# Optimization experiments

Measured on AMD Instinct MI355X. Metric: run time of the kernel, lower is better.

The kernel has to match this reference:

```python
import jax, jax.numpy as jnp
import numpy as np

B, S, D = 16, 1024, 1024  # shape constraints force S == D == 1024


def setup_inputs() -> dict:
    key = jax.random.key(0)
    k1, k2, k3 = jax.random.split(key, 3)
    f1_norm = jax.random.normal(k1, (B, S, D), dtype=jnp.float32)
    f2_norm = jax.random.normal(k2, (B, S, D), dtype=jnp.float32)
    # xavier_normal_ init: std = sqrt(2 / (fan_in + fan_out))
    xavier_std = float(np.sqrt(2.0 / (D + D)))
    corr_weights = jax.random.normal(k3, (D, D), dtype=jnp.float32) * xavier_std
    return {"f1_norm": f1_norm, "f2_norm": f2_norm, "corr_weights": corr_weights}


def reference(f1_norm, f2_norm, corr_weights):
    # a1 = f1 @ W : [B, S, D]
    a1 = jnp.einsum('bsd,de->bse', f1_norm, corr_weights)
    # cc_mat = a1 @ f2^T : [B, S1, S2]
    cc_mat = jnp.einsum('bse,bte->bst', a1, f2_norm)
    audio_att = jax.nn.softmax(cc_mat, axis=1)                      # softmax over S1
    visual_att = jax.nn.softmax(jnp.swapaxes(cc_mat, 1, 2), axis=1)  # [B,S2,S1], softmax over S2
    atten_audiofeatures = jnp.matmul(f1_norm, audio_att)             # [B, S1(=D), S2]
    atten_visualfeatures = jnp.matmul(f2_norm, visual_att)           # [B, S2(=D), S1]
    return (jnp.swapaxes(atten_audiofeatures, 1, 2),
            jnp.swapaxes(atten_visualfeatures, 1, 2))
```

## Files before the change

### kernel.cpp

```cpp
#include <hip/hip_runtime.h>
#include <hip/hip_bf16.h>
#include <stdint.h>

typedef __bf16 bf16_t;
typedef bf16_t bf16x8 __attribute__((ext_vector_type(8)));
typedef bf16_t bf16x4 __attribute__((ext_vector_type(4)));
typedef float  f32x4  __attribute__((ext_vector_type(4)));

#define B_  16
#define S_  1024
#define D_  1024
#define BS_ (B_ * S_)
#define MAT_ (S_ * D_)

#define BAR()   __builtin_amdgcn_s_barrier()
#define LGKM0() asm volatile("s_waitcnt lgkmcnt(0)" ::: "memory")
#define VMC4()  asm volatile("s_waitcnt vmcnt(4)" ::: "memory")

__device__ __forceinline__ void async_load16(const void* g, void* l) {
    __builtin_amdgcn_global_load_lds((__attribute__((address_space(1))) void*)(g),
                                     (__attribute__((address_space(3))) void*)(l),
                                     16, 0, 0);
}

template <int SPLIT, int OSP, int XS>
__global__ __launch_bounds__(512, 2)
void gemm8p(const bf16_t* __restrict__ gAh, const bf16_t* __restrict__ gAl,
            const bf16_t* __restrict__ gBh, const bf16_t* __restrict__ gBl,
            float* __restrict__ Cf, bf16_t* __restrict__ Ch, bf16_t* __restrict__ Cl,
            int M, int N, int K, long sA, long sB, long sC)
{
    (void)M;
    constexpr int BK  = SPLIT ? 32 : 64;
    constexpr int BUF = 65536;
    __shared__ __attribute__((aligned(16))) char smem[2 * BUF];

    const int tid  = threadIdx.x;
    const int w    = tid >> 6;
    const int lane = tid & 63;
    const int wm   = w >> 2;
    const int wn   = w & 3;
    const int fm   = lane & 15;
    const int quad = lane >> 4;

    int bm, bn, b;
    if constexpr (XS) {
        const int flat = (int)blockIdx.x + ((int)blockIdx.y << 2) + ((int)blockIdx.z << 4);
        const int xcd = flat & 7, slot = flat >> 3;
        b  = (xcd << 1) | (slot >> 4);
        bm = (slot >> 2) & 3;
        bn = slot & 3;
    } else {
        bn = blockIdx.x; bm = blockIdx.y; b = blockIdx.z;
    }

    const int NT    = K / BK;
    const int abase = (int)((long)b * sA) + bm * 256 * K;
    const int bbase = (int)((long)b * sB) + bn * 256 * K;

    int aof[2][2], bof[2][2], lof[2][2];
    if constexpr (!SPLIT) {
#pragma unroll
        for (int h = 0; h < 2; ++h)
#pragma unroll
            for (int i = 0; i < 2; ++i) {
                const int o   = h * 16384 + i * 8192 + tid * 16;
                const int row = o >> 7;
                const int c   = ((o >> 4) & 7) ^ (((o >> 9) & 3) << 1);
                aof[h][i] = abase + row * K + c * 8;
                bof[h][i] = bbase + row * K + c * 8;
                lof[h][i] = o;
            }
    } else {
#pragma unroll
        for (int h = 0; h < 2; ++h) {
            const int o   = h * 8192 + tid * 16;
            const int row = o >> 6;
            const int c   = (o >> 4) & 3;
            aof[h][0] = abase + row * K + c * 8;
            bof[h][0] = bbase + row * K + c * 8;
            lof[h][0] = o;
        }
    }

    f32x4 acc[8][4] = {};

    if constexpr (!SPLIT) {
        auto stgA = [&](int t, int h, int lb) {
            const int k = (t < NT ? t : NT - 1) * BK;
            async_load16(gAh + (aof[h][0] + k), smem + lb + lof[h][0]);
            async_load16(gAh + (aof[h][1] + k), smem + lb + lof[h][1]);
        };
        auto stgB = [&](int t, int h, int lb) {
            const int k = (t < NT ? t : NT - 1) * BK;
            async_load16(gBh + (bof[h][0] + k), smem + lb + 32768 + lof[h][0]);
            async_load16(gBh + (bof[h][1] + k), smem + lb + 32768 + lof[h][1]);
        };
        const int xb = ((lane >> 2) & 3) << 5;
        auto ldA = [&](int lb, int m, int ks) -> bf16x8 {
            const int row = wm * 128 + m * 16 + fm;
            return *(const bf16x8*)(smem + lb + row * 128 + ((ks * 64 + quad * 16) ^ xb));
        };
        auto ldB = [&](int lb, int n, int ks) -> bf16x8 {
            const int row = wn * 64 + n * 16 + fm;
            return *(const bf16x8*)(smem + lb + 32768 + row * 128 + ((ks * 64 + quad * 16) ^ xb));
        };

        bf16x8 ar[4][2], br[4][2];
        auto qp = [&](int mh, int nh) {
#pragma unroll
            for (int m = 0; m < 4; ++m)
#pragma unroll
                for (int n = 0; n < 2; ++n) {
                    f32x4 c = acc[mh * 4 + m][nh * 2 + n];
                    c = __builtin_amdgcn_mfma_f32_16x16x32_bf16(ar[m][0], br[nh * 2 + n][0], c, 0, 0, 0);
                    c = __builtin_amdgcn_mfma_f32_16x16x32_bf16(ar[m][1], br[nh * 2 + n][1], c, 0, 0, 0);
                    acc[mh * 4 + m][nh * 2 + n] = c;
                }
        };

        stgA(0, 0, 0); stgA(0, 1, 0); stgB(0, 0, 0); stgB(0, 1, 0);
        stgB(1, 0, BUF); stgB(1, 1, BUF);
        VMC4(); BAR();

        const int NIT = NT >> 1;
        for (int it = 0; it < NIT; ++it) {
            const int t = it << 1;
#pragma unroll
            for (int ph = 0; ph < 2; ++ph) {
                const int rb = ph ? BUF : 0;
                const int ob = ph ? 0 : BUF;
                const int tt = t + ph;
#pragma unroll
                for (int m = 0; m < 4; ++m) { ar[m][0] = ldA(rb, m, 0); ar[m][1] = ldA(rb, m, 1); }
#pragma unroll
                for (int n = 0; n < 2; ++n) { br[n][0] = ldB(rb, n, 0); br[n][1] = ldB(rb, n, 1); }
                stgA(tt + 1, 0, ob);
                BAR(); LGKM0(); __builtin_amdgcn_s_setprio(1);
                qp(0, 0);
                __builtin_amdgcn_s_setprio(0); BAR();
#pragma unroll
                for (int n = 2; n < 4; ++n) { br[n][0] = ldB(rb, n, 0); br[n][1] = ldB(rb, n, 1); }
                stgA(tt + 1, 1, ob);
                BAR(); LGKM0(); __builtin_amdgcn_s_setprio(1);
                qp(0, 1);
                __builtin_amdgcn_s_setprio(0); BAR();
#pragma unroll
                for (int m = 0; m < 4; ++m) { ar[m][0] = ldA(rb, m + 4, 0); ar[m][1] = ldA(rb, m + 4, 1); }
                stgB(tt + 2, 0, rb);
                BAR(); LGKM0(); __builtin_amdgcn_s_setprio(1);
                qp(1, 0);
                __builtin_amdgcn_s_setprio(0); BAR();
                stgB(tt + 2, 1, rb);
                BAR(); LGKM0(); __builtin_amdgcn_s_setprio(1);
                qp(1, 1);
                __builtin_amdgcn_s_setprio(0); VMC4(); BAR();
            }
        }
    } else {
        auto stgAh = [&](int t, int lb) {
            const int k = (t < NT ? t : NT - 1) * BK;
            async_load16(gAh + (aof[0][0] + k), smem + lb + lof[0][0]);
            async_load16(gAh + (aof[1][0] + k), smem + lb + lof[1][0]);
        };
        auto stgAl = [&](int t, int lb) {
            const int k = (t < NT ? t : NT - 1) * BK;
            async_load16(gAl + (aof[0][0] + k), smem + lb + 16384 + lof[0][0]);
            async_load16(gAl + (aof[1][0] + k), smem + lb + 16384 + lof[1][0]);
        };
        auto stgBh = [&](int t, int lb) {
            const int k = (t < NT ? t : NT - 1) * BK;
            async_load16(gBh + (bof[0][0] + k), smem + lb + 32768 + lof[0][0]);
            async_load16(gBh + (bof[1][0] + k), smem + lb + 32768 + lof[1][0]);
        };
        auto stgBl = [&](int t, int lb) {
            const int k = (t < NT ? t : NT - 1) * BK;
            async_load16(gBl + (bof[0][0] + k), smem + lb + 49152 + lof[0][0]);
            async_load16(gBl + (bof[1][0] + k), smem + lb + 49152 + lof[1][0]);
        };
        auto ldSA = [&](int lb, int comp, int m) -> bf16x8 {
            const int row = wm * 128 + m * 16 + fm;
            return *(const bf16x8*)(smem + lb + comp * 16384 + row * 64 + quad * 16);
        };
        auto ldSB = [&](int lb, int comp, int n) -> bf16x8 {
            const int row = wn * 64 + n * 16 + fm;
            return *(const bf16x8*)(smem + lb + comp * 16384 + row * 64 + quad * 16);
        };

        bf16x8 arh[4], arl[4], brh[4], brl[4];
        auto qs = [&](int mh, int nh) {
#pragma unroll
            for (int m = 0; m < 4; ++m)
#pragma unroll
                for (int n = 0; n < 2; ++n) {
                    f32x4 c = acc[mh * 4 + m][nh * 2 + n];
                    c = __builtin_amdgcn_mfma_f32_16x16x32_bf16(arh[m], brh[nh * 2 + n], c, 0, 0, 0);
                    c = __builtin_amdgcn_mfma_f32_16x16x32_bf16(arl[m], brh[nh * 2 + n], c, 0, 0, 0);
                    c = __builtin_amdgcn_mfma_f32_16x16x32_bf16(arh[m], brl[nh * 2 + n], c, 0, 0, 0);
                    acc[mh * 4 + m][nh * 2 + n] = c;
                }
        };

        stgAh(0, 0); stgAl(0, 0); stgBh(0, 0); stgBl(0, 0);
        stgBh(1, BUF); stgBl(1, BUF);
        VMC4(); BAR();

        const int NIT = NT >> 1;
        for (int it = 0; it < NIT; ++it) {
            const int t = it << 1;
#pragma unroll
            for (int ph = 0; ph < 2; ++ph) {
                const int rb = ph ? BUF : 0;
                const int ob = ph ? 0 : BUF;
                const int tt = t + ph;
#pragma unroll
                for (int m = 0; m < 4; ++m) { arh[m] = ldSA(rb, 0, m); arl[m] = ldSA(rb, 1, m); }
#pragma unroll
                for (int n = 0; n < 2; ++n) { brh[n] = ldSB(rb, 2, n); brl[n] = ldSB(rb, 3, n); }
                stgAh(tt + 1, ob);
                BAR(); LGKM0(); __builtin_amdgcn_s_setprio(1);
                qs(0, 0);
                __builtin_amdgcn_s_setprio(0); BAR();
#pragma unroll
                for (int n = 2; n < 4; ++n) { brh[n] = ldSB(rb, 2, n); brl[n] = ldSB(rb, 3, n); }
                stgAl(tt + 1, ob);
                BAR(); LGKM0(); __builtin_amdgcn_s_setprio(1);
                qs(0, 1);
                __builtin_amdgcn_s_setprio(0); BAR();
#pragma unroll
                for (int m = 0; m < 4; ++m) { arh[m] = ldSA(rb, 0, m + 4); arl[m] = ldSA(rb, 1, m + 4); }
                stgBh(tt + 2, rb);
                BAR(); LGKM0(); __builtin_amdgcn_s_setprio(1);
                qs(1, 0);
                __builtin_amdgcn_s_setprio(0); BAR();
                stgBl(tt + 2, rb);
                BAR(); LGKM0(); __builtin_amdgcn_s_setprio(1);
                qs(1, 1);
                __builtin_amdgcn_s_setprio(0); VMC4(); BAR();
            }
        }
    }

#pragma unroll
    for (int i = 0; i < 8; ++i) {
        const int row0 = bm * 256 + wm * 128 + i * 16 + quad * 4;
#pragma unroll
        for (int j = 0; j < 4; ++j) {
            const int col = bn * 256 + wn * 64 + j * 16 + fm;
#pragma unroll
            for (int r = 0; r < 4; ++r) {
                const long idx = (long)b * sC + (long)(row0 + r) * N + col;
                const float v = acc[i][j][r];
                if constexpr (OSP) {
                    const bf16_t h = (bf16_t)v;
                    Ch[idx] = h;
                    Cl[idx] = (bf16_t)(v - (float)h);
                } else {
                    Cf[idx] = v;
                }
            }
        }
    }
}

__global__ void split_f32(const float* __restrict__ s,
                          bf16_t* __restrict__ h, bf16_t* __restrict__ l)
{
    const long i = ((long)blockIdx.x * 256 + threadIdx.x) * 4;
    float4 v = *(const float4*)(s + i);
    float a[4] = {v.x, v.y, v.z, v.w};
    bf16x4 hh, ll;
#pragma unroll
    for (int e = 0; e < 4; ++e) {
        const bf16_t hv = (bf16_t)a[e];
        hh[e] = hv;
        ll[e] = (bf16_t)(a[e] - (float)hv);
    }
    *(bf16x4*)(h + i) = hh;
    *(bf16x4*)(l + i) = ll;
}

__global__ void transpose_split_w(const float* __restrict__ W,
                                  bf16_t* __restrict__ Wth, bf16_t* __restrict__ Wtl)
{
    __shared__ float tile[32][33];
    const int d0 = blockIdx.x * 32, e0 = blockIdx.y * 32;
    const int tx = threadIdx.x, ty = threadIdx.y;
    for (int r = ty; r < 32; r += 8)
        tile[r][tx] = W[(long)(d0 + r) * D_ + e0 + tx];
    __syncthreads();
    for (int r = ty; r < 32; r += 8) {
        const float v = tile[tx][r];
        const bf16_t h = (bf16_t)v;
        Wth[(long)(e0 + r) * D_ + d0 + tx] = h;
        Wtl[(long)(e0 + r) * D_ + d0 + tx] = (bf16_t)(v - (float)h);
    }
}

__global__ void col_stats_partial(const float* __restrict__ cc,
                                  float* __restrict__ Mp, float* __restrict__ Zp)
{
    const int b = blockIdx.x, tc = blockIdx.y, sc = blockIdx.z;
    const int t = tc * 256 + threadIdx.x;
    const float* p = cc + (long)b * MAT_ + (long)sc * 128 * S_ + t;
    float m = p[0], z = 1.f;
    for (int s = 1; s < 128; ++s) {
        float v = p[(long)s * S_];
        float nm = fmaxf(m, v);
        z = z * __expf(m - nm) + __expf(v - nm);
        m = nm;
    }
    const int idx = ((b * 8 + sc) << 10) + t;
    Mp[idx] = m; Zp[idx] = z;
}

__global__ void col_stats_combine(const float* __restrict__ Mp, const float* __restrict__ Zp,
                                  float* __restrict__ Mst, float* __restrict__ Zst)
{
    const int i = blockIdx.x * 256 + threadIdx.x;
    const int b = i >> 10, t = i & 1023;
    float m = Mp[((b * 8) << 10) + t], z = Zp[((b * 8) << 10) + t];
    for (int c = 1; c < 8; ++c) {
        float mc = Mp[((b * 8 + c) << 10) + t];
        float zc = Zp[((b * 8 + c) << 10) + t];
        float nm = fmaxf(m, mc);
        z = z * __expf(m - nm) + zc * __expf(mc - nm);
        m = nm;
    }
    Mst[i] = m; Zst[i] = z;
}

__global__ void row_stats(const float* __restrict__ cc,
                          float* __restrict__ Nst, float* __restrict__ Yst)
{
    const int row  = (blockIdx.x * 256 + threadIdx.x) >> 6;
    const int lane = threadIdx.x & 63;
    const float* p = cc + (long)row * S_;
    float m = p[lane], z = 1.f;
    for (int j = 1; j < 16; ++j) {
        float v = p[lane + j * 64];
        float nm = fmaxf(m, v);
        z = z * __expf(m - nm) + __expf(v - nm);
        m = nm;
    }
    for (int off = 32; off > 0; off >>= 1) {
        float mo = __shfl_down(m, off);
        float zo = __shfl_down(z, off);
        float nm = fmaxf(m, mo);
        z = z * __expf(m - nm) + zo * __expf(mo - nm);
        m = nm;
    }
    if (lane == 0) { Nst[row] = m; Yst[row] = z; }
}

__global__ void build_atts(const float* __restrict__ cc,
                           const float* __restrict__ Mst, const float* __restrict__ Zst,
                           const float* __restrict__ Nst, const float* __restrict__ Yst,
                           bf16_t* __restrict__ attA, bf16_t* __restrict__ attV)
{
    __shared__ float tile[32][33];
    const int b = blockIdx.z;
    const int s0 = blockIdx.x * 32, t0 = blockIdx.y * 32;
    const int tx = threadIdx.x, ty = threadIdx.y;
    const float* src = cc + (long)b * MAT_;
    bf16_t* dV = attV + (long)b * MAT_;
    bf16_t* dA = attA + (long)b * MAT_;
    for (int r = ty; r < 32; r += 8) {
        const int s = s0 + r;
        const float v = src[(long)s * S_ + t0 + tx];
        tile[r][tx] = v;
        dV[(long)s * S_ + t0 + tx] =
            (bf16_t)(__expf(v - Nst[b * 1024 + s]) * (1.f / Yst[b * 1024 + s]));
    }
    __syncthreads();
    for (int r = ty; r < 32; r += 8) {
        const int t = t0 + r;
        const float m  = Mst[b * 1024 + t];
        const float rz = 1.f / Zst[b * 1024 + t];
        dA[(long)t * S_ + s0 + tx] = (bf16_t)(__expf(tile[tx][r] - m) * rz);
    }
}

extern "C" void kernel_launch(void* const* d_in, const int* in_sizes, int n_in,
                              void* d_out, int out_size, void* d_ws, size_t ws_size,
                              hipStream_t stream)
{
    const float* f1 = (const float*)d_in[0];
    const float* f2 = (const float*)d_in[1];
    const float* W  = (const float*)d_in[2];

    float* out0 = (float*)d_out;
    float* out1 = out0 + (long)B_ * MAT_;

    bf16_t* a1h = (bf16_t*)out0;
    bf16_t* a1l = a1h + (long)B_ * MAT_;
    bf16_t* Wth = (bf16_t*)out1;
    bf16_t* Wtl = Wth + (long)MAT_;
    float*  cc  = out1;

    char* w = (char*)d_ws;
    bf16_t* f1h  = (bf16_t*)(w);
    bf16_t* f2h  = (bf16_t*)(w + (32l << 20));
    bf16_t* f1l  = (bf16_t*)(w + (64l << 20));
    bf16_t* f2l  = (bf16_t*)(w + (96l << 20));
    bf16_t* attA = f1l;
    bf16_t* attV = f2l;
    float*  Mp   = (float*)(w + (128l << 20));
    float*  Zp   = Mp + 16 * 8 * 1024;
    float*  Mst  = Zp + 16 * 8 * 1024;
    float*  Zst  = Mst + BS_;
    float*  Nst  = Zst + BS_;
    float*  Yst  = Nst + BS_;

    split_f32<<<16384, 256, 0, stream>>>(f1, f1h, f1l);
    split_f32<<<16384, 256, 0, stream>>>(f2, f2h, f2l);
    transpose_split_w<<<dim3(32, 32), dim3(32, 8), 0, stream>>>(W, Wth, Wtl);

    gemm8p<1, 1, 0><<<dim3(4, 64, 1), 512, 0, stream>>>(
        f1h, f1l, Wth, Wtl, nullptr, a1h, a1l, BS_, 1024, 1024, 0, 0, 0);

    gemm8p<1, 0, 1><<<dim3(4, 4, 16), 512, 0, stream>>>(
        a1h, a1l, f2h, f2l, cc, nullptr, nullptr, 1024, 1024, 1024, MAT_, MAT_, MAT_);

    col_stats_partial<<<dim3(16, 4, 8), 256, 0, stream>>>(cc, Mp, Zp);
    col_stats_combine<<<64, 256, 0, stream>>>(Mp, Zp, Mst, Zst);
    row_stats<<<4096, 256, 0, stream>>>(cc, Nst, Yst);

    build_atts<<<dim3(32, 32, 16), dim3(32, 8), 0, stream>>>(
        cc, Mst, Zst, Nst, Yst, attA, attV);

    gemm8p<0, 0, 1><<<dim3(4, 4, 16), 512, 0, stream>>>(
        attA, nullptr, f1h, nullptr, out0, nullptr, nullptr,
        1024, 1024, 1024, MAT_, MAT_, MAT_);

    gemm8p<0, 0, 1><<<dim3(4, 4, 16), 512, 0, stream>>>(
        attV, nullptr, f2h, nullptr, out1, nullptr, nullptr,
        1024, 1024, 1024, MAT_, MAT_, MAT_);
}
```

Baseline: 565.2 us.

## Fuse softmax stats into GEMM epilogue, merge launches, and re-swizzle LDS

```diff
diff --git a/kernel.cpp b/kernel.cpp
--- a/kernel.cpp
+++ b/kernel.cpp
@@ -23,11 +23,13 @@
                                      16, 0, 0);
 }
 
-template <int SPLIT, int OSP, int XS>
+template <int SPLIT, int OSP, int XS, int STATS>
 __global__ __launch_bounds__(512, 2)
 void gemm8p(const bf16_t* __restrict__ gAh, const bf16_t* __restrict__ gAl,
             const bf16_t* __restrict__ gBh, const bf16_t* __restrict__ gBl,
             float* __restrict__ Cf, bf16_t* __restrict__ Ch, bf16_t* __restrict__ Cl,
+            float* __restrict__ Mp2, float* __restrict__ Zp2,
+            float* __restrict__ Np2, float* __restrict__ Yp2,
             int M, int N, int K, long sA, long sB, long sC)
 {
     (void)M;
@@ -44,14 +46,33 @@
     const int quad = lane >> 4;
 
     int bm, bn, b;
-    if constexpr (XS) {
+    if constexpr (XS == 1) {
         const int flat = (int)blockIdx.x + ((int)blockIdx.y << 2) + ((int)blockIdx.z << 4);
         const int xcd = flat & 7, slot = flat >> 3;
         b  = (xcd << 1) | (slot >> 4);
         bm = (slot >> 2) & 3;
         bn = slot & 3;
+    } else if constexpr (XS == 2) {
+        const int flat = (int)blockIdx.x + ((int)blockIdx.y << 2) + ((int)blockIdx.z << 4);
+        const int xcd = flat & 7, slot = flat >> 3;
+        b  = (xcd << 2) | (slot >> 4);
+        bm = (slot >> 2) & 3;
+        bn = slot & 3;
+    } else if constexpr (XS == 3) {
+        const int flat = (int)blockIdx.x + ((int)blockIdx.y << 2);
+        const int xcd = flat & 7, slot = flat >> 3;
+        b  = 0;
+        bm = (xcd << 3) | (slot >> 2);
+        bn = slot & 3;
     } else {
         bn = blockIdx.x; bm = blockIdx.y; b = blockIdx.z;
+    }
+
+    const bf16_t* pAh = gAh; const bf16_t* pAl = gAl;
+    const bf16_t* pBh = gBh; const bf16_t* pBl = gBl;
+    float* Cfp = Cf;
+    if constexpr (XS == 2) {
+        if (b >= 16) { pAh = gAl; pBh = gBl; Cfp = Cf + (long)B_ * MAT_; b -= 16; }
     }
 
     const int NT    = K / BK;
@@ -66,7 +87,7 @@
             for (int i = 0; i < 2; ++i) {
                 const int o   = h * 16384 + i * 8192 + tid * 16;
                 const int row = o >> 7;
-                const int c   = ((o >> 4) & 7) ^ (((o >> 9) & 3) << 1);
+                const int c   = ((o >> 4) & 7) ^ (row & 7);
                 aof[h][i] = abase + row * K + c * 8;
                 bof[h][i] = bbase + row * K + c * 8;
                 lof[h][i] = o;
@@ -76,7 +97,7 @@
         for (int h = 0; h < 2; ++h) {
             const int o   = h * 8192 + tid * 16;
             const int row = o >> 6;
-            const int c   = (o >> 4) & 3;
+            const int c   = ((o >> 4) & 3) ^ ((row >> 1) & 3);
             aof[h][0] = abase + row * K + c * 8;
             bof[h][0] = bbase + row * K + c * 8;
             lof[h][0] = o;
@@ -88,15 +109,15 @@
     if constexpr (!SPLIT) {
         auto stgA = [&](int t, int h, int lb) {
             const int k = (t < NT ? t : NT - 1) * BK;
-            async_load16(gAh + (aof[h][0] + k), smem + lb + lof[h][0]);
-            async_load16(gAh + (aof[h][1] + k), smem + lb + lof[h][1]);
+            async_load16(pAh + (aof[h][0] + k), smem + lb + lof[h][0]);
+            async_load16(pAh + (aof[h][1] + k), smem + lb + lof[h][1]);
         };
         auto stgB = [&](int t, int h, int lb) {
             const int k = (t < NT ? t : NT - 1) * BK;
-            async_load16(gBh + (bof[h][0] + k), smem + lb + 32768 + lof[h][0]);
-            async_load16(gBh + (bof[h][1] + k), smem + lb + 32768 + lof[h][1]);
-        };
-        const int xb = ((lane >> 2) & 3) << 5;
+            async_load16(pBh + (bof[h][0] + k), smem + lb + 32768 + lof[h][0]);
+            async_load16(pBh + (bof[h][1] + k), smem + lb + 32768 + lof[h][1]);
+        };
+        const int xb = (fm & 7) << 4;
         auto ldA = [&](int lb, int m, int ks) -> bf16x8 {
             const int row = wm * 128 + m * 16 + fm;
             return *(const bf16x8*)(smem + lb + row * 128 + ((ks * 64 + quad * 16) ^ xb));
@@ -160,31 +181,32 @@
     } else {
         auto stgAh = [&](int t, int lb) {
             const int k = (t < NT ? t : NT - 1) * BK;
-            async_load16(gAh + (aof[0][0] + k), smem + lb + lof[0][0]);
-            async_load16(gAh + (aof[1][0] + k), smem + lb + lof[1][0]);
+            async_load16(pAh + (aof[0][0] + k), smem + lb + lof[0][0]);
+            async_load16(pAh + (aof[1][0] + k), smem + lb + lof[1][0]);
         };
         auto stgAl = [&](int t, int lb) {
             const int k = (t < NT ? t : NT - 1) * BK;
-            async_load16(gAl + (aof[0][0] + k), smem + lb + 16384 + lof[0][0]);
-            async_load16(gAl + (aof[1][0] + k), smem + lb + 16384 + lof[1][0]);
+            async_load16(pAl + (aof[0][0] + k), smem + lb + 16384 + lof[0][0]);
+            async_load16(pAl + (aof[1][0] + k), smem + lb + 16384 + lof[1][0]);
         };
         auto stgBh = [&](int t, int lb) {
             const int k = (t < NT ? t : NT - 1) * BK;
-            async_load16(gBh + (bof[0][0] + k), smem + lb + 32768 + lof[0][0]);
-            async_load16(gBh + (bof[1][0] + k), smem + lb + 32768 + lof[1][0]);
+            async_load16(pBh + (bof[0][0] + k), smem + lb + 32768 + lof[0][0]);
+            async_load16(pBh + (bof[1][0] + k), smem + lb + 32768 + lof[1][0]);
         };
         auto stgBl = [&](int t, int lb) {
             const int k = (t < NT ? t : NT - 1) * BK;
-            async_load16(gBl + (bof[0][0] + k), smem + lb + 49152 + lof[0][0]);
-            async_load16(gBl + (bof[1][0] + k), smem + lb + 49152 + lof[1][0]);
-        };
+            async_load16(pBl + (bof[0][0] + k), smem + lb + 49152 + lof[0][0]);
+            async_load16(pBl + (bof[1][0] + k), smem + lb + 49152 + lof[1][0]);
+        };
+        const int xs2 = ((fm >> 1) & 3) << 4;
         auto ldSA = [&](int lb, int comp, int m) -> bf16x8 {
             const int row = wm * 128 + m * 16 + fm;
-            return *(const bf16x8*)(smem + lb + comp * 16384 + row * 64 + quad * 16);
+            return *(const bf16x8*)(smem + lb + comp * 16384 + row * 64 + ((quad * 16) ^ xs2));
         };
         auto ldSB = [&](int lb, int comp, int n) -> bf16x8 {
             const int row = wn * 64 + n * 16 + fm;
-            return *(const bf16x8*)(smem + lb + comp * 16384 + row * 64 + quad * 16);
+            return *(const bf16x8*)(smem + lb + comp * 16384 + row * 64 + ((quad * 16) ^ xs2));
         };
 
         bf16x8 arh[4], arl[4], brh[4], brl[4];
@@ -239,6 +261,48 @@
                 __builtin_amdgcn_s_setprio(0); VMC4(); BAR();
             }
         }
+    }
+
+    float2* colp = (float2*)smem;
+    float2* rowp = (float2*)(smem + 4096);
+    if constexpr (STATS) {
+#pragma unroll
+        for (int j = 0; j < 4; ++j) {
+            float m = acc[0][j][0];
+#pragma unroll
+            for (int i = 0; i < 8; ++i)
+#pragma unroll
+                for (int r = 0; r < 4; ++r) m = fmaxf(m, acc[i][j][r]);
+            float z = 0.f;
+#pragma unroll
+            for (int i = 0; i < 8; ++i)
+#pragma unroll
+                for (int r = 0; r < 4; ++r) z += __expf(acc[i][j][r] - m);
+#pragma unroll
+            for (int off = 16; off <= 32; off <<= 1) {
+                float mo = __shfl_xor(m, off), zo = __shfl_xor(z, off);
+                float nm = fmaxf(m, mo);
+                z = z * __expf(m - nm) + zo * __expf(mo - nm); m = nm;
+            }
+            if (quad == 0) colp[wm * 256 + wn * 64 + j * 16 + fm] = make_float2(m, z);
+        }
+#pragma unroll
+        for (int i = 0; i < 8; ++i)
+#pragma unroll
+            for (int r = 0; r < 4; ++r) {
+                float m = fmaxf(fmaxf(acc[i][0][r], acc[i][1][r]),
+                                fmaxf(acc[i][2][r], acc[i][3][r]));
+                float z = __expf(acc[i][0][r] - m) + __expf(acc[i][1][r] - m)
+                        + __expf(acc[i][2][r] - m) + __expf(acc[i][3][r] - m);
+#pragma unroll
+                for (int off = 1; off <= 8; off <<= 1) {
+                    float mo = __shfl_xor(m, off), zo = __shfl_xor(z, off);
+                    float nm = fmaxf(m, mo);
+                    z = z * __expf(m - nm) + zo * __expf(mo - nm); m = nm;
+                }
+                if (fm == 0)
+                    rowp[wn * 256 + wm * 128 + i * 16 + quad * 4 + r] = make_float2(m, z);
+            }
     }
 
 #pragma unroll
@@ -256,17 +320,47 @@
                     Ch[idx] = h;
                     Cl[idx] = (bf16_t)(v - (float)h);
                 } else {
-                    Cf[idx] = v;
+                    Cfp[idx] = v;
                 }
             }
         }
     }
-}
-
-__global__ void split_f32(const float* __restrict__ s,
-                          bf16_t* __restrict__ h, bf16_t* __restrict__ l)
-{
-    const long i = ((long)blockIdx.x * 256 + threadIdx.x) * 4;
+
+    if constexpr (STATS) {
+        __syncthreads();
+        if (tid < 256) {
+            float2 p0 = colp[tid], p1 = colp[256 + tid];
+            float nm = fmaxf(p0.x, p1.x);
+            float z = p0.y * __expf(p0.x - nm) + p1.y * __expf(p1.x - nm);
+            const int gcol = bn * 256 + tid;
+            Mp2[((b * 4 + bm) << 10) + gcol] = nm;
+            Zp2[((b * 4 + bm) << 10) + gcol] = z;
+        } else {
+            const int rr = tid - 256;
+            float2 p = rowp[rr];
+            float m = p.x, z = p.y;
+#pragma unroll
+            for (int c = 1; c < 4; ++c) {
+                float2 q = rowp[c * 256 + rr];
+                float nm = fmaxf(m, q.x);
+                z = z * __expf(m - nm) + q.y * __expf(q.x - nm); m = nm;
+            }
+            const int grow = bm * 256 + rr;
+            Np2[((b * 4 + bn) << 10) + grow] = m;
+            Yp2[((b * 4 + bn) << 10) + grow] = z;
+        }
+    }
+}
+
+__global__ void split2_f32(const float* __restrict__ f1, const float* __restrict__ f2,
+                           bf16_t* __restrict__ h1, bf16_t* __restrict__ l1,
+                           bf16_t* __restrict__ h2, bf16_t* __restrict__ l2)
+{
+    const long tot = (long)B_ * MAT_;
+    long i = ((long)blockIdx.x * 256 + threadIdx.x) * 4;
+    const float* s; bf16_t* h; bf16_t* l;
+    if (i < tot) { s = f1; h = h1; l = l1; }
+    else { i -= tot; s = f2; h = h2; l = l2; }
     float4 v = *(const float4*)(s + i);
     float a[4] = {v.x, v.y, v.z, v.w};
     bf16x4 hh, ll;
@@ -297,60 +391,27 @@
     }
 }
 
-__global__ void col_stats_partial(const float* __restrict__ cc,
-                                  float* __restrict__ Mp, float* __restrict__ Zp)
-{
-    const int b = blockIdx.x, tc = blockIdx.y, sc = blockIdx.z;
-    const int t = tc * 256 + threadIdx.x;
-    const float* p = cc + (long)b * MAT_ + (long)sc * 128 * S_ + t;
-    float m = p[0], z = 1.f;
-    for (int s = 1; s < 128; ++s) {
-        float v = p[(long)s * S_];
-        float nm = fmaxf(m, v);
-        z = z * __expf(m - nm) + __expf(v - nm);
-        m = nm;
-    }
-    const int idx = ((b * 8 + sc) << 10) + t;
-    Mp[idx] = m; Zp[idx] = z;
-}
-
-__global__ void col_stats_combine(const float* __restrict__ Mp, const float* __restrict__ Zp,
-                                  float* __restrict__ Mst, float* __restrict__ Zst)
+__global__ void combine_stats(const float* __restrict__ Mp2, const float* __restrict__ Zp2,
+                              const float* __restrict__ Np2, const float* __restrict__ Yp2,
+                              float* __restrict__ Mst, float* __restrict__ Zst,
+                              float* __restrict__ Nst, float* __restrict__ Yst)
 {
     const int i = blockIdx.x * 256 + threadIdx.x;
-    const int b = i >> 10, t = i & 1023;
-    float m = Mp[((b * 8) << 10) + t], z = Zp[((b * 8) << 10) + t];
-    for (int c = 1; c < 8; ++c) {
-        float mc = Mp[((b * 8 + c) << 10) + t];
-        float zc = Zp[((b * 8 + c) << 10) + t];
+    const int which = i >> 14;
+    const int idx = i & 16383;
+    const int b = idx >> 10, x = idx & 1023;
+    const float* P = which ? Np2 : Mp2;
+    const float* Q = which ? Yp2 : Zp2;
+    const int base = (b << 12) + x;
+    float m = P[base], z = Q[base];
+#pragma unroll
+    for (int c = 1; c < 4; ++c) {
+        float mc = P[base + (c << 10)], zc = Q[base + (c << 10)];
         float nm = fmaxf(m, mc);
-        z = z * __expf(m - nm) + zc * __expf(mc - nm);
-        m = nm;
-    }
-    Mst[i] = m; Zst[i] = z;
-}
-
-__global__ void row_stats(const float* __restrict__ cc,
-                          float* __restrict__ Nst, float* __restrict__ Yst)
-{
-    const int row  = (blockIdx.x * 256 + threadIdx.x) >> 6;
-    const int lane = threadIdx.x & 63;
-    const float* p = cc + (long)row * S_;
-    float m = p[lane], z = 1.f;
-    for (int j = 1; j < 16; ++j) {
-        float v = p[lane + j * 64];
-        float nm = fmaxf(m, v);
-        z = z * __expf(m - nm) + __expf(v - nm);
-        m = nm;
-    }
-    for (int off = 32; off > 0; off >>= 1) {
-        float mo = __shfl_down(m, off);
-        float zo = __shfl_down(z, off);
-        float nm = fmaxf(m, mo);
-        z = z * __expf(m - nm) + zo * __expf(mo - nm);
-        m = nm;
-    }
-    if (lane == 0) { Nst[row] = m; Yst[row] = z; }
+        z = z * __expf(m - nm) + zc * __expf(mc - nm); m = nm;
+    }
+    if (which) { Nst[idx] = m; Yst[idx] = z; }
+    else       { Mst[idx] = m; Zst[idx] = z; }
 }
 
 __global__ void build_atts(const float* __restrict__ cc,
@@ -405,35 +466,32 @@
     bf16_t* f2l  = (bf16_t*)(w + (96l << 20));
     bf16_t* attA = f1l;
     bf16_t* attV = f2l;
-    float*  Mp   = (float*)(w + (128l << 20));
-    float*  Zp   = Mp + 16 * 8 * 1024;
-    float*  Mst  = Zp + 16 * 8 * 1024;
+    float*  Mp2  = (float*)(w + (128l << 20));
+    float*  Zp2  = Mp2 + 16 * 4 * 1024;
+    float*  Np2  = Zp2 + 16 * 4 * 1024;
+    float*  Yp2  = Np2 + 16 * 4 * 1024;
+    float*  Mst  = Yp2 + 16 * 4 * 1024;
     float*  Zst  = Mst + BS_;
     float*  Nst  = Zst + BS_;
     float*  Yst  = Nst + BS_;
 
-    split_f32<<<16384, 256, 0, stream>>>(f1, f1h, f1l);
-    split_f32<<<16384, 256, 0, stream>>>(f2, f2h, f2l);
+    split2_f32<<<32768, 256, 0, stream>>>(f1, f2, f1h, f1l, f2h, f2l);
     transpose_split_w<<<dim3(32, 32), dim3(32, 8), 0, stream>>>(W, Wth, Wtl);
 
-    gemm8p<1, 1, 0><<<dim3(4, 64, 1), 512, 0, stream>>>(
-        f1h, f1l, Wth, Wtl, nullptr, a1h, a1l, BS_, 1024, 1024, 0, 0, 0);
-
-    gemm8p<1, 0, 1><<<dim3(4, 4, 16), 512, 0, stream>>>(
-        a1h, a1l, f2h, f2l, cc, nullptr, nullptr, 1024, 1024, 1024, MAT_, MAT_, MAT_);
-
-    col_stats_partial<<<dim3(16, 4, 8), 256, 0, stream>>>(cc, Mp, Zp);
-    col_stats_combine<<<64, 256, 0, stream>>>(Mp, Zp, Mst, Zst);
-    row_stats<<<4096, 256, 0, stream>>>(cc, Nst, Yst);
+    gemm8p<1, 1, 3, 0><<<dim3(4, 64, 1), 512, 0, stream>>>(
+        f1h, f1l, Wth, Wtl, nullptr, a1h, a1l,
+        nullptr, nullptr, nullptr, nullptr, BS_, 1024, 1024, 0, 0, 0);
+
+    gemm8p<1, 0, 1, 1><<<dim3(4, 4, 16), 512, 0, stream>>>(
+        a1h, a1l, f2h, f2l, cc, nullptr, nullptr,
+        Mp2, Zp2, Np2, Yp2, 1024, 1024, 1024, MAT_, MAT_, MAT_);
+
+    combine_stats<<<128, 256, 0, stream>>>(Mp2, Zp2, Np2, Yp2, Mst, Zst, Nst, Yst);
 
     build_atts<<<dim3(32, 32, 16), dim3(32, 8), 0, stream>>>(
         cc, Mst, Zst, Nst, Yst, attA, attV);
 
-    gemm8p<0, 0, 1><<<dim3(4, 4, 16), 512, 0, stream>>>(
-        attA, nullptr, f1h, nullptr, out0, nullptr, nullptr,
-        1024, 1024, 1024, MAT_, MAT_, MAT_);
-
-    gemm8p<0, 0, 1><<<dim3(4, 4, 16), 512, 0, stream>>>(
-        attV, nullptr, f2h, nullptr, out1, nullptr, nullptr,
-        1024, 1024, 1024, MAT_, MAT_, MAT_);
-}
+    gemm8p<0, 0, 2, 0><<<dim3(4, 4, 32), 512, 0, stream>>>(
+        attA, attV, f1h, f2h, out0, nullptr, nullptr,
+        nullptr, nullptr, nullptr, nullptr, 1024, 1024, 1024, MAT_, MAT_, MAT_);
+}
```

Result: faster. 504.8 us (-10.7%).
